# Optimization experiments

Hardware: AMD Instinct MI355X
Metric: run time of the kernel (lower is better)

## Reference

```python
import jax, jax.numpy as jnp
import numpy as np

SCALING = 32.0 / 16.0  # lora_alpha / lora_rank


def setup_inputs() -> dict:
    key = jax.random.key(0)
    ks = jax.random.split(key, 6)
    B_, S, D, O, E, R = 4, 2048, 4096, 4096, 8, 16
    x = jax.random.normal(ks[0], (B_, S, D), dtype=jnp.float32)
    W_base = jax.random.normal(ks[1], (O, D), dtype=jnp.float32) * (D ** -0.5)
    b_base = jax.random.normal(ks[2], (O,), dtype=jnp.float32) * 0.01
    W_gate = jax.random.normal(ks[3], (E, D), dtype=jnp.float32) * (D ** -0.5)
    A = jax.random.normal(ks[4], (E, R, D), dtype=jnp.float32) * (D ** -0.5)
    B = jax.random.normal(ks[5], (O, R), dtype=jnp.float32)[None] * (R ** -0.5)
    B = jnp.broadcast_to(B, (E, O, R)) * jnp.linspace(0.5, 1.5, E)[:, None, None]
    return {"x": x, "W_base": W_base, "b_base": b_base, "W_gate": W_gate,
            "A": A, "B": B, "top_k": 2}


def reference(x, W_base, b_base, W_gate, A, B, top_k):
    D = x.shape[-1]
    O = W_base.shape[0]
    E = W_gate.shape[0]
    xf = x.reshape(-1, D)                      # [N, D] flattened tokens
    N = xf.shape[0]

    # base linear
    base = jnp.einsum('nd,od->no', xf, W_base) + b_base          # [N, O]

    # gating: softmax then top-k, renormalize selected weights
    gate_logits = jax.nn.softmax(xf @ W_gate.T, axis=-1)          # [N, E]
    w, sel = jax.lax.top_k(gate_logits, top_k)                    # [N, k]
    w = w / jnp.sum(w, axis=-1, keepdims=True)

    # dense per-(token, expert) weight; non-selected experts get 0,
    # equivalent to the scatter-add combine in the original code.
    w_dense = jnp.zeros((N, E), dtype=x.dtype).at[
        jnp.arange(N)[:, None], sel].set(w)                       # [N, E]

    # LoRA expert compute: down-proj for every expert (rank is small),
    # weight, then up-proj and combine across experts.
    h = jnp.einsum('nd,erd->ner', xf, A)                          # [N, E, R]
    hw = h * w_dense[:, :, None]                                  # [N, E, R]
    moe = jnp.einsum('ner,eor->no', hw, B) * SCALING              # [N, O]

    out = (base + moe).reshape(x.shape[:-1] + (O,))
    return out
```

## Files before the change

### kernel.cpp

```cpp
#include <hip/hip_runtime.h>
#include <stdint.h>

typedef unsigned short u16;
typedef float f32x4 __attribute__((ext_vector_type(4)));
typedef short bf16x8 __attribute__((ext_vector_type(8)));

static __device__ __forceinline__ u16 f2bf(float f) {
  union { float f; unsigned u; } a; a.f = f;
  unsigned r = a.u + 0x7fffu + ((a.u >> 16) & 1u);
  return (u16)(r >> 16);
}

static __device__ __forceinline__ void gld16(const void* g, void* l) {
  __builtin_amdgcn_global_load_lds(
      (const __attribute__((address_space(1))) void*)(uintptr_t)g,
      (__attribute__((address_space(3))) void*)(uintptr_t)l,
      16, 0, 0);
}

__global__ __launch_bounds__(256) void fused_pre(
    const float* __restrict__ x, const float* __restrict__ Wg,
    const float* __restrict__ Wb, const float* __restrict__ B,
    const float* __restrict__ A,
    u16* __restrict__ Xaug, u16* __restrict__ Waug, u16* __restrict__ a2,
    float* __restrict__ wsc) {
  const int bid = blockIdx.x;
  const int t = threadIdx.x;
  if (bid < 2048) {
    const int lane = t & 63;
    const int wv = t >> 6;
    const int n = bid * 4 + wv;
    const float4* x4 = (const float4*)(x + (size_t)n * 4096);
    const float4* g4 = (const float4*)Wg;
    u16* xr = Xaug + (size_t)n * 4224;
    float acc[8] = {0, 0, 0, 0, 0, 0, 0, 0};
#pragma unroll
    for (int ii = 0; ii < 16; ++ii) {
      const int i = ii * 64 + lane;
      float4 xv = x4[i];
      ushort4 o;
      o.x = f2bf(xv.x); o.y = f2bf(xv.y); o.z = f2bf(xv.z); o.w = f2bf(xv.w);
      *(ushort4*)(xr + i * 4) = o;
#pragma unroll
      for (int e = 0; e < 8; ++e) {
        float4 w4 = g4[e * 1024 + i];
        acc[e] += xv.x * w4.x + xv.y * w4.y + xv.z * w4.z + xv.w * w4.w;
      }
    }
#pragma unroll
    for (int e = 0; e < 8; ++e) {
#pragma unroll
      for (int off = 32; off > 0; off >>= 1)
        acc[e] += __shfl_xor(acc[e], off);
    }
    int i1 = 0; float m1 = acc[0];
#pragma unroll
    for (int e = 1; e < 8; ++e) if (acc[e] > m1) { m1 = acc[e]; i1 = e; }
    int i2 = -1; float m2 = -3.4e38f;
#pragma unroll
    for (int e = 0; e < 8; ++e) if (e != i1 && acc[e] > m2) { m2 = acc[e]; i2 = e; }
    float w1 = 1.0f / (1.0f + expf(m2 - m1));
    float w2 = 1.0f - w1;
    if (lane < 8)
      wsc[(size_t)n * 8 + lane] = (lane == i1) ? w1 : ((lane == i2) ? w2 : 0.0f);
  } else if (bid < 4096) {
    const int total = 4096 * 1056;
    for (int v = (bid - 2048) * 256 + t; v < total; v += 2048 * 256) {
      const int o = v / 1056;
      const int c = (v - o * 1056) * 4;
      ushort4 out;
      if (c < 4096) {
        float4 w = *(const float4*)(Wb + (size_t)o * 4096 + c);
        out.x = f2bf(w.x); out.y = f2bf(w.y); out.z = f2bf(w.z); out.w = f2bf(w.w);
      } else {
        const int er = c - 4096;
        const int e = er >> 4;
        const int r = er & 15;
        const float* bp = B + ((size_t)e * 4096 + o) * 16 + r;
        out.x = f2bf(bp[0] * 2.0f); out.y = f2bf(bp[1] * 2.0f);
        out.z = f2bf(bp[2] * 2.0f); out.w = f2bf(bp[3] * 2.0f);
      }
      *(ushort4*)(Waug + (size_t)o * 4224 + c) = out;
    }
  } else {
    const int i = (bid - 4096) * 256 + t;
    const size_t e = (size_t)i * 4;
    float4 v = *(const float4*)(A + e);
    ushort4 o;
    o.x = f2bf(v.x); o.y = f2bf(v.y); o.z = f2bf(v.z); o.w = f2bf(v.w);
    *(ushort4*)(a2 + e) = o;
  }
}

__global__ __launch_bounds__(256) void lora_hw(
    const u16* __restrict__ Xa, const u16* __restrict__ A2,
    const float* __restrict__ wsc, u16* __restrict__ Xaug) {
  __shared__ __align__(1024) char lds[20480];
  const int t = threadIdx.x;
  const int lane = t & 63;
  const int w = t >> 6;
  const int l15 = lane & 15, lhi = lane >> 4;
  const int brow = blockIdx.x * 32;

  const int sb = (lane << 4) ^ (lane & 32);
  const int srow = sb >> 6;
  const int scol = (sb & 63) >> 1;

  const u16* pA = Xa + (size_t)(brow + (w >> 1) * 16 + srow) * 4224 + (w & 1) * 32 + scol;
  const u16* pB[4];
#pragma unroll
  for (int s = 0; s < 4; ++s) {
    const int idx = w * 4 + s;
    pB[s] = A2 + (size_t)((idx >> 1) * 16 + srow) * 4096 + (idx & 1) * 32 + scol;
  }
  const int dA = w << 10;
  const int dB = 4096 + (w << 12);

  const int innerL = ((l15 << 6) + (lhi << 4)) ^ ((l15 & 8) << 2);

  f32x4 acc[2][2] = {};

  for (int k0 = 0; k0 < 4096; k0 += 64) {
    gld16(pA + k0, lds + dA);
#pragma unroll
    for (int s = 0; s < 4; ++s) gld16(pB[s] + k0, lds + dB + (s << 10));
    __syncthreads();
    bf16x8 av[2][2], bv[2][2];
#pragma unroll
    for (int m = 0; m < 2; ++m)
#pragma unroll
      for (int kk = 0; kk < 2; ++kk)
        av[m][kk] = *(const bf16x8*)(lds + ((m * 2 + kk) << 10) + innerL);
#pragma unroll
    for (int n = 0; n < 2; ++n)
#pragma unroll
      for (int kk = 0; kk < 2; ++kk)
        bv[n][kk] = *(const bf16x8*)(lds + 4096 + (((w * 2 + n) * 2 + kk) << 10) + innerL);
#pragma unroll
    for (int kk = 0; kk < 2; ++kk)
#pragma unroll
      for (int m = 0; m < 2; ++m)
#pragma unroll
        for (int n = 0; n < 2; ++n)
          acc[m][n] = __builtin_amdgcn_mfma_f32_16x16x32_bf16(av[m][kk], bv[n][kk], acc[m][n], 0, 0, 0);
    __syncthreads();
  }
#pragma unroll
  for (int m = 0; m < 2; ++m) {
    const int rbase = brow + m * 16 + lhi * 4;
#pragma unroll
    for (int n = 0; n < 2; ++n) {
      const int col = w * 32 + n * 16 + l15;
#pragma unroll
      for (int j = 0; j < 4; ++j) {
        const int row = rbase + j;
        const float g = wsc[(size_t)row * 8 + (col >> 4)];
        Xaug[(size_t)row * 4224 + 4096 + col] = f2bf(acc[m][n][j] * g);
      }
    }
  }
}

#define BAR do { asm volatile("" ::: "memory"); __builtin_amdgcn_s_barrier(); asm volatile("" ::: "memory"); } while (0)

#define RDA(BUF, MH)                                                            \
  { _Pragma("unroll") for (int mm = 0; mm < 4; ++mm)                            \
    _Pragma("unroll") for (int kk = 0; kk < 2; ++kk)                            \
      av[mm][kk] = *(const bf16x8*)(lds + (BUF) + fbA + ((((MH) * 4 + mm) * 2 + kk) << 10)); }

#define RDB(BUF, NH)                                                            \
  { _Pragma("unroll") for (int nn = 0; nn < 2; ++nn)                            \
    _Pragma("unroll") for (int kk = 0; kk < 2; ++kk)                            \
      bv[(NH) * 2 + nn][kk] = *(const bf16x8*)(lds + (BUF) + fbB + ((((NH) * 2 + nn) * 2 + kk) << 10)); }

#define MFMAQ(MH, NH)                                                           \
  { __builtin_amdgcn_s_setprio(1);                                              \
    _Pragma("unroll") for (int kk = 0; kk < 2; ++kk)                            \
    _Pragma("unroll") for (int mm = 0; mm < 4; ++mm)                            \
    _Pragma("unroll") for (int nn = 0; nn < 2; ++nn)                            \
      acc[(MH) * 4 + mm][(NH) * 2 + nn] = __builtin_amdgcn_mfma_f32_16x16x32_bf16( \
          av[mm][kk], bv[(NH) * 2 + nn][kk], acc[(MH) * 4 + mm][(NH) * 2 + nn], 0, 0, 0); \
    __builtin_amdgcn_s_setprio(0); }

__global__ __launch_bounds__(512, 2) void gemm8p(
    const u16* __restrict__ Ag, const u16* __restrict__ Bg,
    const float* __restrict__ bias, float* __restrict__ C,
    int lda, int ldb, int ldc, int K) {
  __shared__ __align__(1024) char lds[131072];
  const int t = threadIdx.x;
  const int lane = t & 63;
  const int w = t >> 6;
  const int wr = w >> 2, wc = w & 3;
  const int l15 = lane & 15, lhi = lane >> 4;

  const int bid = blockIdx.x;
  const int g = bid >> 3;
  const int tile_m = (bid & 7) * 4 + (g & 3);
  const int tile_n = g >> 2;
  const int brow = tile_m << 8;
  const int bcol = tile_n << 8;

  const int sb = (lane << 4) ^ (lane & 32);
  const int srow = sb >> 6;
  const int scol = (sb & 63) >> 1;

  const u16* pA[4]; const u16* pB[4];
#pragma unroll
  for (int s = 0; s < 4; ++s) {
    const int idx = w * 4 + s;
    const int rg = idx >> 1, cs = idx & 1;
    pA[s] = Ag + (size_t)(brow + rg * 16 + srow) * lda + cs * 32 + scol;
    pB[s] = Bg + (size_t)(bcol + rg * 16 + srow) * ldb + cs * 32 + scol;
  }
  const int ldsA = w << 12;
  const int ldsB = 32768 + (w << 12);

  const int innerL = ((l15 << 6) + (lhi << 4)) ^ ((l15 & 8) << 2);
  const int fbA = (wr << 14) + innerL;
  const int fbB = 32768 + (wc << 13) + innerL;

  f32x4 acc[8][4] = {};
  bf16x8 av[4][2], bv[4][2];

  const int NT = K >> 6;

#pragma unroll
  for (int s = 0; s < 4; ++s) gld16(pA[s], lds + ldsA + (s << 10));
#pragma unroll
  for (int s = 0; s < 4; ++s) gld16(pB[s], lds + ldsB + (s << 10));
#pragma unroll
  for (int s = 0; s < 4; ++s) gld16(pB[s] + 64, lds + 65536 + ldsB + (s << 10));
#pragma unroll
  for (int s = 0; s < 4; ++s) { pA[s] += 64; pB[s] += 128; }
  asm volatile("s_waitcnt vmcnt(4)" ::: "memory");
  BAR;
  RDA(0, 0); RDB(0, 0);

  for (int j = 0; j < NT; ++j) {
    const int buf  = (j & 1) << 16;
    const int obuf = buf ^ 65536;
    const bool stA = (j + 1 < NT);
    const bool stB = (j + 2 < NT);
    if (stA) { gld16(pA[0], lds + obuf + ldsA);
               gld16(pA[1], lds + obuf + ldsA + 1024); }
    MFMAQ(0, 0);
    RDB(buf, 1);
    BAR;
    if (stA) { gld16(pA[2], lds + obuf + ldsA + 2048);
               gld16(pA[3], lds + obuf + ldsA + 3072); }
    MFMAQ(0, 1);
    RDA(buf, 1);
    BAR;
    if (stB) { gld16(pB[0], lds + buf + ldsB);
               gld16(pB[1], lds + buf + ldsB + 1024); }
    MFMAQ(1, 1);
    BAR;
    if (stB) { gld16(pB[2], lds + buf + ldsB + 2048);
               gld16(pB[3], lds + buf + ldsB + 3072); }
    if (j < NT - 2)       { asm volatile("s_waitcnt vmcnt(4)" ::: "memory"); }
    else if (j == NT - 2) { asm volatile("s_waitcnt vmcnt(0)" ::: "memory"); }
    BAR;
    MFMAQ(1, 0);
    if (stA) { RDA(obuf, 0); RDB(obuf, 0); }
#pragma unroll
    for (int s = 0; s < 4; ++s) { pA[s] += 64; pB[s] += 64; }
  }

#pragma unroll
  for (int m = 0; m < 8; ++m) {
    const int row0 = brow + wr * 128 + m * 16 + lhi * 4;
#pragma unroll
    for (int n = 0; n < 4; ++n) {
      const int col = bcol + wc * 64 + n * 16 + l15;
      const float b2 = bias[col];
#pragma unroll
      for (int jj = 0; jj < 4; ++jj)
        C[(size_t)(row0 + jj) * ldc + col] = acc[m][n][jj] + b2;
    }
  }
}

extern "C" void kernel_launch(void* const* d_in, const int* in_sizes, int n_in,
                              void* d_out, int out_size, void* d_ws, size_t ws_size,
                              hipStream_t stream) {
  const float* x  = (const float*)d_in[0];
  const float* Wb = (const float*)d_in[1];
  const float* bb = (const float*)d_in[2];
  const float* Wg = (const float*)d_in[3];
  const float* A  = (const float*)d_in[4];
  const float* B  = (const float*)d_in[5];
  float* out = (float*)d_out;

  char* ws = (char*)d_ws;
  u16*   Xaug = (u16*)ws;
  u16*   Waug = (u16*)(ws + 69206016);
  u16*   a2   = (u16*)(ws + 69206016 + 34603008);
  float* wsc  = (float*)(ws + 69206016 + 34603008 + 1048576);

  fused_pre<<<4608, 256, 0, stream>>>(x, Wg, Wb, B, A, Xaug, Waug, a2, wsc);

  lora_hw<<<256, 256, 0, stream>>>(Xaug, a2, wsc, Xaug);

  gemm8p<<<512, 512, 0, stream>>>(Xaug, Waug, bb, out, 4224, 4224, 4096, 4224);
}
```

Baseline: 385.4 us.

## Double-buffer LoRA down-proj loads and batch four tokens per wave in gating

The lora_hw kernel now double-buffers its LDS tiles and prefetches the next K-slice with global_load_lds while computing on the current one, using explicit vmcnt waits. This is meant to hide global-load latency in that small-grid kernel. The gating/convert part of fused_pre now has each wave process four tokens, so every W_gate load is reused across four tokens and fewer blocks are launched. The cost is doubled LDS use in lora_hw and more registers per thread in fused_pre.

New measurement: 595.7 us. +54.6%, slower.

```diff
diff --git a/kernel.cpp b/kernel.cpp
--- a/kernel.cpp
+++ b/kernel.cpp
@@ -26,46 +26,57 @@
     float* __restrict__ wsc) {
   const int bid = blockIdx.x;
   const int t = threadIdx.x;
-  if (bid < 2048) {
+  if (bid < 512) {
     const int lane = t & 63;
     const int wv = t >> 6;
-    const int n = bid * 4 + wv;
-    const float4* x4 = (const float4*)(x + (size_t)n * 4096);
+    const int n0 = bid * 16 + wv * 4;
     const float4* g4 = (const float4*)Wg;
-    u16* xr = Xaug + (size_t)n * 4224;
-    float acc[8] = {0, 0, 0, 0, 0, 0, 0, 0};
+    float acc[4][8] = {};
 #pragma unroll
     for (int ii = 0; ii < 16; ++ii) {
       const int i = ii * 64 + lane;
-      float4 xv = x4[i];
-      ushort4 o;
-      o.x = f2bf(xv.x); o.y = f2bf(xv.y); o.z = f2bf(xv.z); o.w = f2bf(xv.w);
-      *(ushort4*)(xr + i * 4) = o;
+      float4 xv[4];
+#pragma unroll
+      for (int tok = 0; tok < 4; ++tok) {
+        xv[tok] = *(const float4*)(x + (size_t)(n0 + tok) * 4096 + i * 4);
+        ushort4 o;
+        o.x = f2bf(xv[tok].x); o.y = f2bf(xv[tok].y);
+        o.z = f2bf(xv[tok].z); o.w = f2bf(xv[tok].w);
+        *(ushort4*)(Xaug + (size_t)(n0 + tok) * 4224 + i * 4) = o;
+      }
 #pragma unroll
       for (int e = 0; e < 8; ++e) {
         float4 w4 = g4[e * 1024 + i];
-        acc[e] += xv.x * w4.x + xv.y * w4.y + xv.z * w4.z + xv.w * w4.w;
-      }
-    }
-#pragma unroll
-    for (int e = 0; e < 8; ++e) {
-#pragma unroll
-      for (int off = 32; off > 0; off >>= 1)
-        acc[e] += __shfl_xor(acc[e], off);
-    }
-    int i1 = 0; float m1 = acc[0];
-#pragma unroll
-    for (int e = 1; e < 8; ++e) if (acc[e] > m1) { m1 = acc[e]; i1 = e; }
-    int i2 = -1; float m2 = -3.4e38f;
-#pragma unroll
-    for (int e = 0; e < 8; ++e) if (e != i1 && acc[e] > m2) { m2 = acc[e]; i2 = e; }
-    float w1 = 1.0f / (1.0f + expf(m2 - m1));
-    float w2 = 1.0f - w1;
-    if (lane < 8)
-      wsc[(size_t)n * 8 + lane] = (lane == i1) ? w1 : ((lane == i2) ? w2 : 0.0f);
-  } else if (bid < 4096) {
+#pragma unroll
+        for (int tok = 0; tok < 4; ++tok)
+          acc[tok][e] += xv[tok].x * w4.x + xv[tok].y * w4.y +
+                         xv[tok].z * w4.z + xv[tok].w * w4.w;
+      }
+    }
+#pragma unroll
+    for (int tok = 0; tok < 4; ++tok) {
+#pragma unroll
+      for (int e = 0; e < 8; ++e) {
+#pragma unroll
+        for (int off = 32; off > 0; off >>= 1)
+          acc[tok][e] += __shfl_xor(acc[tok][e], off);
+      }
+      int i1 = 0; float m1 = acc[tok][0];
+#pragma unroll
+      for (int e = 1; e < 8; ++e) if (acc[tok][e] > m1) { m1 = acc[tok][e]; i1 = e; }
+      int i2 = -1; float m2 = -3.4e38f;
+#pragma unroll
+      for (int e = 0; e < 8; ++e)
+        if (e != i1 && acc[tok][e] > m2) { m2 = acc[tok][e]; i2 = e; }
+      float w1 = 1.0f / (1.0f + expf(m2 - m1));
+      float w2 = 1.0f - w1;
+      if (lane < 8)
+        wsc[(size_t)(n0 + tok) * 8 + lane] =
+            (lane == i1) ? w1 : ((lane == i2) ? w2 : 0.0f);
+    }
+  } else if (bid < 2560) {
     const int total = 4096 * 1056;
-    for (int v = (bid - 2048) * 256 + t; v < total; v += 2048 * 256) {
+    for (int v = (bid - 512) * 256 + t; v < total; v += 2048 * 256) {
       const int o = v / 1056;
       const int c = (v - o * 1056) * 4;
       ushort4 out;
@@ -83,7 +94,7 @@
       *(ushort4*)(Waug + (size_t)o * 4224 + c) = out;
     }
   } else {
-    const int i = (bid - 4096) * 256 + t;
+    const int i = (bid - 2560) * 256 + t;
     const size_t e = (size_t)i * 4;
     float4 v = *(const float4*)(A + e);
     ushort4 o;
@@ -95,7 +106,7 @@
 __global__ __launch_bounds__(256) void lora_hw(
     const u16* __restrict__ Xa, const u16* __restrict__ A2,
     const float* __restrict__ wsc, u16* __restrict__ Xaug) {
-  __shared__ __align__(1024) char lds[20480];
+  __shared__ __align__(1024) char lds[40960];
   const int t = threadIdx.x;
   const int lane = t & 63;
   const int w = t >> 6;
@@ -120,22 +131,34 @@
 
   f32x4 acc[2][2] = {};
 
-  for (int k0 = 0; k0 < 4096; k0 += 64) {
-    gld16(pA + k0, lds + dA);
-#pragma unroll
-    for (int s = 0; s < 4; ++s) gld16(pB[s] + k0, lds + dB + (s << 10));
+  gld16(pA, lds + dA);
+#pragma unroll
+  for (int s = 0; s < 4; ++s) gld16(pB[s], lds + dB + (s << 10));
+
+  for (int j = 0; j < 64; ++j) {
+    const int buf = (j & 1) * 20480;
+    const int obuf = buf ^ 20480;
+    if (j < 63) {
+      const int k1 = (j + 1) * 64;
+      gld16(pA + k1, lds + obuf + dA);
+#pragma unroll
+      for (int s = 0; s < 4; ++s) gld16(pB[s] + k1, lds + obuf + dB + (s << 10));
+      asm volatile("s_waitcnt vmcnt(5)" ::: "memory");
+    } else {
+      asm volatile("s_waitcnt vmcnt(0)" ::: "memory");
+    }
     __syncthreads();
     bf16x8 av[2][2], bv[2][2];
 #pragma unroll
     for (int m = 0; m < 2; ++m)
 #pragma unroll
       for (int kk = 0; kk < 2; ++kk)
-        av[m][kk] = *(const bf16x8*)(lds + ((m * 2 + kk) << 10) + innerL);
+        av[m][kk] = *(const bf16x8*)(lds + buf + ((m * 2 + kk) << 10) + innerL);
 #pragma unroll
     for (int n = 0; n < 2; ++n)
 #pragma unroll
       for (int kk = 0; kk < 2; ++kk)
-        bv[n][kk] = *(const bf16x8*)(lds + 4096 + (((w * 2 + n) * 2 + kk) << 10) + innerL);
+        bv[n][kk] = *(const bf16x8*)(lds + buf + 4096 + (((w * 2 + n) * 2 + kk) << 10) + innerL);
 #pragma unroll
     for (int kk = 0; kk < 2; ++kk)
 #pragma unroll
@@ -297,7 +320,7 @@
   u16*   a2   = (u16*)(ws + 69206016 + 34603008);
   float* wsc  = (float*)(ws + 69206016 + 34603008 + 1048576);
 
-  fused_pre<<<4608, 256, 0, stream>>>(x, Wg, Wb, B, A, Xaug, Waug, a2, wsc);
+  fused_pre<<<3072, 256, 0, stream>>>(x, Wg, Wb, B, A, Xaug, Waug, a2, wsc);
 
   lora_hw<<<256, 256, 0, stream>>>(Xaug, a2, wsc, Xaug);
 
```
